# Optimization experiments

Hardware: AMD Instinct MI355X
Metric: run time of the kernel (lower is better)

## Reference

```python
import jax, jax.numpy as jnp
import numpy as np

K = 30  # kNN neighbors (DynamicEdgeConvParams default)

def _knn_idx(x, k):
    # x: [B,N,C] -> indices of k nearest neighbors in feature space, [B,N,k]
    x2 = jnp.sum(x * x, axis=-1)                      # [B,N]
    d = x2[:, :, None] + x2[:, None, :] - 2.0 * jnp.einsum('bnc,bmc->bnm', x, x)
    _, idx = jax.lax.top_k(-d, k)                     # includes self (dist 0)
    return idx

def _edge_conv(x, w0, b0, w1, b1, k):
    # DynamicEdgeConv: kNN on x, edge feat [x_i, x_j - x_i], MLP, max-aggr
    idx = _knn_idx(x, k)                              # [B,N,k]
    xj = jax.vmap(lambda xb, ib: xb[ib])(x, idx)      # [B,N,k,C] gather
    xi = jnp.broadcast_to(x[:, :, None, :], xj.shape)
    e = jnp.concatenate([xi, xj - xi], axis=-1)       # [B,N,k,2C]
    h = jax.nn.relu(jnp.einsum('bnkc,cd->bnkd', e, w0) + b0)
    h = jnp.einsum('bnkc,cd->bnkd', h, w1) + b1
    return jnp.max(h, axis=2)                         # [B,N,out]

def setup_inputs() -> dict:
    key = jax.random.key(0)
    ks = jax.random.split(key, 16)
    def w(k, shape):
        fan_in = shape[0]
        return jax.random.normal(k, shape, jnp.float32) / np.sqrt(fan_in)
    B, N = 16, 2048
    return {
        'pos': jax.random.normal(ks[0], (B, N, 3), jnp.float32),
        'c1_w0': w(ks[1], (6, 64)),   'c1_b0': jnp.zeros((64,), jnp.float32),
        'c1_w1': w(ks[2], (64, 64)),  'c1_b1': jnp.zeros((64,), jnp.float32),
        'c2_w0': w(ks[3], (128, 64)), 'c2_b0': jnp.zeros((64,), jnp.float32),
        'c2_w1': w(ks[4], (64, 64)),  'c2_b1': jnp.zeros((64,), jnp.float32),
        'c3_w0': w(ks[5], (128, 64)), 'c3_b0': jnp.zeros((64,), jnp.float32),
        'c3_w1': w(ks[6], (64, 64)),  'c3_b1': jnp.zeros((64,), jnp.float32),
        'mlp_w0': w(ks[7], (192, 1024)), 'mlp_b0': jnp.zeros((1024,), jnp.float32),
        'mlp_w1': w(ks[8], (1024, 256)), 'mlp_b1': jnp.zeros((256,), jnp.float32),
        'mlp_w2': w(ks[9], (256, 128)),  'mlp_b2': jnp.zeros((128,), jnp.float32),
        'fin_w': w(ks[10], (128, 3)),    'fin_b': jnp.zeros((3,), jnp.float32),
    }

def reference(pos, c1_w0, c1_b0, c1_w1, c1_b1, c2_w0, c2_b0, c2_w1, c2_b1,
              c3_w0, c3_b0, c3_w1, c3_b1, mlp_w0, mlp_b0, mlp_w1, mlp_b1,
              mlp_w2, mlp_b2, fin_w, fin_b):
    x1 = _edge_conv(pos, c1_w0, c1_b0, c1_w1, c1_b1, K)   # [B,N,64]
    x2 = _edge_conv(x1, c2_w0, c2_b0, c2_w1, c2_b1, K)    # [B,N,64]
    x3 = _edge_conv(x2, c3_w0, c3_b0, c3_w1, c3_b1, K)    # [B,N,64]
    h = jnp.concatenate([x1, x2, x3], axis=-1)            # [B,N,192]
    h = jax.nn.relu(h @ mlp_w0 + mlp_b0)
    h = jax.nn.relu(h @ mlp_w1 + mlp_b1)
    h = h @ mlp_w2 + mlp_b2                               # [B,N,128]
    return h @ fin_w + fin_b                              # [B,N,3]
```

## Files before the change

### kernel.cpp

```cpp
#include <hip/hip_runtime.h>
#include <hip/hip_bf16.h>
#include <cfloat>
#include <cstddef>

#define BB 16
#define NN 2048
#define KNN 30
#define MC 8192

using bf16 = __hip_bfloat16;
typedef short short8 __attribute__((ext_vector_type(8)));
typedef float floatx4 __attribute__((ext_vector_type(4)));

constexpr size_t XT_O  = 0;
constexpr size_t NRM_O = XT_O  + (size_t)BB*64*NN;
constexpr size_t A_O   = NRM_O + (size_t)BB*NN;
constexpr size_t U_O   = A_O   + (size_t)BB*NN*64;
constexpr size_t H_O   = U_O   + (size_t)BB*NN*64;
constexpr size_t WS_F  = H_O   + (size_t)BB*NN*192;
constexpr size_t H1C_S = 0;
constexpr size_t H2C_S = 8388608;
constexpr size_t WB_S  = 11534336;
constexpr size_t WB1_S = WB_S + 0;
constexpr size_t WB2_S = WB_S + 196608;
constexpr size_t WB3_S = WB_S + 458752;

__device__ __attribute__((aligned(16))) float g_ws[WS_F];
__device__ int   g_idx[(size_t)BB*NN*KNN];
__device__ int   g_isbf16;

__device__ __forceinline__ float b2f(bf16 x){ return __bfloat162float(x); }
__device__ __forceinline__ float ldi(const void* p, size_t i){
  return g_isbf16 ? b2f(((const bf16*)p)[i]) : ((const float*)p)[i];
}
__device__ __forceinline__ short f2bs(float v){
  bf16 h = __float2bfloat16(v);
  return *reinterpret_cast<short*>(&h);
}
__device__ __forceinline__ float bs2f(short s){
  bf16 h = *reinterpret_cast<bf16*>(&s);
  return __bfloat162float(h);
}
__device__ __forceinline__ unsigned fmono(float x){
  unsigned u = __float_as_uint(x);
  return ((int)u < 0) ? ~u : (u | 0x80000000u);
}

__global__ __launch_bounds__(256) void k_sniff(const unsigned* __restrict__ posw){
  __shared__ int cnt[256];
  const int tid = threadIdx.x;
  int c = 0;
  for(int k=0;k<8;k++){
    unsigned w = posw[tid*8+k];
    unsigned code = (w & 0x7F80u) >> 7;
    if(code >= 119u && code <= 129u) c++;
  }
  cnt[tid] = c; __syncthreads();
  for(int s=128;s>0;s>>=1){ if(tid<s) cnt[tid]+=cnt[tid+s]; __syncthreads(); }
  if(tid==0) g_isbf16 = (cnt[0] > 1024) ? 1 : 0;
}

__global__ __launch_bounds__(256) void k_diag(bf16* __restrict__ out, int n, float v){
  int t = blockIdx.x*256 + threadIdx.x;
  if(t < n) out[t] = __float2bfloat16(v);
}

__global__ __launch_bounds__(256) void k_prep(const void* __restrict__ pos){
  int t = blockIdx.x*256 + threadIdx.x;
  int b = t >> 11, i = t & (NN-1);
  float x = ldi(pos, (size_t)t*3+0), y = ldi(pos, (size_t)t*3+1), z = ldi(pos, (size_t)t*3+2);
  float* Xb = g_ws + XT_O + (size_t)b*64*NN;
  Xb[0*NN+i] = x; Xb[1*NN+i] = y; Xb[2*NN+i] = z;
  g_ws[NRM_O + t] = x*x + y*y + z*z;
}

template<int C, bool EXTIN>
__global__ __launch_bounds__(512, 4) void k_knn_pre(const void* __restrict__ Xin,
    int rowStride, int colOff, const void* __restrict__ W0, const void* __restrict__ b0,
    int xOff){
  constexpr int SM_KNN = 4*NN*4;
  constexpr int SM_PRE = C*64*4*2 + 256;
  constexpr int SMB = SM_KNN > SM_PRE ? SM_KNN : SM_PRE;
  __shared__ __attribute__((aligned(16))) char smem[SMB];
  const int tid = threadIdx.x;
  const int wid = tid >> 6, lane = tid & 63;
  const int bidx = blockIdx.x;

  if(bidx >= 4096){
    float* Wd = (float*)smem;
    float* Wb = Wd + C*64;
    float* bb = Wb + C*64;
    for(int t=tid; t<C*64; t+=512){
      float top = ldi(W0, t), bot = ldi(W0, (size_t)C*64 + t);
      Wd[t] = top - bot; Wb[t] = bot;
    }
    if(tid < 64) bb[tid] = ldi(b0, tid);
    __syncthreads();
    const int pbase = (bidx - 4096)*64 + wid*8;
    float bl = bb[lane];
    float a[8], u[8];
    #pragma unroll
    for(int pp=0;pp<8;pp++){ a[pp] = bl; u[pp] = 0.f; }
    for(int c=0;c<C;c++){
      float wd = Wd[c*64 + lane];
      float wb = Wb[c*64 + lane];
      #pragma unroll
      for(int pp=0;pp<8;pp++){
        float xc;
        if(EXTIN) xc = ldi(Xin, (size_t)(pbase+pp)*rowStride + colOff + c);
        else      xc = g_ws[(size_t)xOff + (size_t)(pbase+pp)*rowStride + colOff + c];
        a[pp] = fmaf(xc, wd, a[pp]);
        u[pp] = fmaf(xc, wb, u[pp]);
      }
    }
    #pragma unroll
    for(int pp=0;pp<8;pp++){
      g_ws[A_O + (size_t)(pbase+pp)*64 + lane] = a[pp];
      g_ws[U_O + (size_t)(pbase+pp)*64 + lane] = u[pp];
    }
    return;
  }

  unsigned (*dlds)[NN] = (unsigned(*)[NN])smem;
  const int b    = bidx >> 8;
  const int i0   = (bidx & 255) * 8;
  const size_t gi0 = (size_t)b*NN + i0;
  const float* Xb  = g_ws + XT_O + (size_t)b*64*NN;
  const float* nrm = g_ws + NRM_O;

  const int j0 = tid*4;
  float4 nj4 = *(const float4*)&nrm[(size_t)b*NN + j0];

  float acc[8][4];
  #pragma unroll
  for(int r=0;r<8;r++)
    #pragma unroll
    for(int s=0;s<4;s++) acc[r][s] = 0.f;

  constexpr int CH  = (C == 3) ? 3 : 2;
  constexpr int NCH = C / CH;
  float4 vb[2][CH];
  #pragma unroll
  for(int cc=0; cc<CH; cc++) vb[0][cc] = *(const float4*)&Xb[(size_t)cc*NN + j0];
  #pragma unroll
  for(int k=0; k<NCH; k++){
    if(k+1 < NCH){
      #pragma unroll
      for(int cc=0; cc<CH; cc++)
        vb[(k+1)&1][cc] = *(const float4*)&Xb[(size_t)((k+1)*CH+cc)*NN + j0];
    }
    #pragma unroll
    for(int cc=0; cc<CH; cc++){
      const int c = k*CH + cc;
      const float4 vj = vb[k&1][cc];
      const float* xr = &Xb[(size_t)c*NN + i0];
      #pragma unroll
      for(int r=0;r<8;r++){
        float xc = xr[r];
        acc[r][0] = fmaf(xc, vj.x, acc[r][0]);
        acc[r][1] = fmaf(xc, vj.y, acc[r][1]);
        acc[r][2] = fmaf(xc, vj.z, acc[r][2]);
        acc[r][3] = fmaf(xc, vj.w, acc[r][3]);
      }
    }
  }

  #pragma unroll
  for(int r=0;r<4;r++){
    float nIr = nrm[gi0 + r];
    uint4 kv;
    kv.x = fmono(fmaf(-2.f, acc[r][0], nIr + nj4.x));
    kv.y = fmono(fmaf(-2.f, acc[r][1], nIr + nj4.y));
    kv.z = fmono(fmaf(-2.f, acc[r][2], nIr + nj4.z));
    kv.w = fmono(fmaf(-2.f, acc[r][3], nIr + nj4.w));
    *(uint4*)&dlds[r][j0] = kv;
  }
  __syncthreads();
  unsigned kk[32];
  if(wid < 4){
    const unsigned* drow = dlds[wid];
    #pragma unroll
    for(int q=0;q<32;q++) kk[q] = drow[lane + (q<<6)];
  }
  __syncthreads();
  #pragma unroll
  for(int r=4;r<8;r++){
    float nIr = nrm[gi0 + r];
    uint4 kv;
    kv.x = fmono(fmaf(-2.f, acc[r][0], nIr + nj4.x));
    kv.y = fmono(fmaf(-2.f, acc[r][1], nIr + nj4.y));
    kv.z = fmono(fmaf(-2.f, acc[r][2], nIr + nj4.z));
    kv.w = fmono(fmaf(-2.f, acc[r][3], nIr + nj4.w));
    *(uint4*)&dlds[r-4][j0] = kv;
  }
  __syncthreads();
  if(wid >= 4){
    const unsigned* drow = dlds[wid-4];
    #pragma unroll
    for(int q=0;q<32;q++) kk[q] = drow[lane + (q<<6)];
  }

  const size_t rowbase = (gi0 + wid)*KNN;

  unsigned lo = 0x80000000u, hi = 0xFFFFFFFFu;
  unsigned T = 0; bool exact = false;
  while(hi - lo > 1u){
    unsigned mid = lo + ((hi - lo) >> 1);
    int tot = 0;
    #pragma unroll
    for(int q=0;q<32;q++) tot += (int)__popcll(__ballot(kk[q] < mid));
    if(tot == KNN){ T = mid; exact = true; break; }
    if(tot < KNN) lo = mid; else hi = mid;
  }

  int base = 0;
  if(exact){
    #pragma unroll
    for(int q=0;q<32;q++){
      bool p = kk[q] < T;
      unsigned long long m = __ballot(p);
      if(p){
        int pos = base + __builtin_amdgcn_mbcnt_hi((unsigned)(m>>32),
                        __builtin_amdgcn_mbcnt_lo((unsigned)m, 0u));
        g_idx[rowbase + pos] = lane + (q<<6);
      }
      base += (int)__popcll(m);
    }
  } else {
    #pragma unroll
    for(int q=0;q<32;q++){
      bool p = kk[q] < lo;
      unsigned long long m = __ballot(p);
      if(p){
        int pos = base + __builtin_amdgcn_mbcnt_hi((unsigned)(m>>32),
                        __builtin_amdgcn_mbcnt_lo((unsigned)m, 0u));
        g_idx[rowbase + pos] = lane + (q<<6);
      }
      base += (int)__popcll(m);
    }
    #pragma unroll
    for(int q=0;q<32;q++){
      bool p = kk[q] == lo;
      unsigned long long m = __ballot(p);
      if(p){
        int pos = base + __builtin_amdgcn_mbcnt_hi((unsigned)(m>>32),
                        __builtin_amdgcn_mbcnt_lo((unsigned)m, 0u));
        if(pos < KNN) g_idx[rowbase + pos] = lane + (q<<6);
      }
      base += (int)__popcll(m);
    }
  }
}

template<bool WRITE_NEXT>
__global__ __launch_bounds__(256) void k_edge_agg(const void* __restrict__ W1,
    const void* __restrict__ b1, int colOff){
  __shared__ short hk_hi[4][32][64] __attribute__((aligned(16)));
  __shared__ short hk_lo[4][32][64] __attribute__((aligned(16)));
  const int tid = threadIdx.x;
  const int wid = tid >> 6, lane = tid & 63;
  const int ml = lane & 15, kgl = lane >> 4;
  short8 wh[2][4], wl[2][4];
  #pragma unroll
  for(int kt=0; kt<2; kt++)
    #pragma unroll
    for(int nt=0; nt<4; nt++)
      #pragma unroll
      for(int j=0; j<8; j++){
        float w = ldi(W1, (size_t)(kt*32 + kgl*8 + j)*64 + nt*16 + ml);
        short hi = f2bs(w);
        wh[kt][nt][j] = hi;
        wl[kt][nt][j] = f2bs(w - bs2f(hi));
      }
  const float bias = ldi(b1, lane);
  hk_hi[wid][30][lane] = 0; hk_hi[wid][31][lane] = 0;
  hk_lo[wid][30][lane] = 0; hk_lo[wid][31][lane] = 0;
  for(int pp=0; pp<4; pp++){
    const int point = blockIdx.x*16 + wid*4 + pp;
    const int b = point >> 11, i = point & (NN-1);
    const float a = g_ws[A_O + (size_t)point*64 + lane];
    const int* ip = g_idx + (size_t)point*KNN;
    const float* Ub = g_ws + U_O + (size_t)b*NN*64;
    int jv = 0;
    if(lane < KNN) jv = ip[lane] & (NN-1);
    #pragma unroll
    for(int kk=0; kk<KNN; kk++){
      int j = __shfl(jv, kk, 64);
      float h = fmaxf(a + Ub[(size_t)j*64 + lane], 0.f);
      short hi = f2bs(h);
      hk_hi[wid][kk][lane] = hi;
      hk_lo[wid][kk][lane] = f2bs(h - bs2f(hi));
    }
    floatx4 acc[2][4];
    #pragma unroll
    for(int t=0;t<2;t++)
      #pragma unroll
      for(int nt=0;nt<4;nt++) acc[t][nt] = (floatx4){0.f,0.f,0.f,0.f};
    #pragma unroll
    for(int t=0;t<2;t++){
      #pragma unroll
      for(int kt=0;kt<2;kt++){
        short8 ah = *(const short8*)&hk_hi[wid][t*16+ml][kt*32 + kgl*8];
        short8 al = *(const short8*)&hk_lo[wid][t*16+ml][kt*32 + kgl*8];
        #pragma unroll
        for(int nt=0;nt<4;nt++){
          acc[t][nt] = __builtin_amdgcn_mfma_f32_16x16x32_bf16(ah, wh[kt][nt], acc[t][nt], 0,0,0);
          acc[t][nt] = __builtin_amdgcn_mfma_f32_16x16x32_bf16(ah, wl[kt][nt], acc[t][nt], 0,0,0);
          acc[t][nt] = __builtin_amdgcn_mfma_f32_16x16x32_bf16(al, wh[kt][nt], acc[t][nt], 0,0,0);
        }
      }
    }
    float cmax[4];
    #pragma unroll
    for(int nt=0;nt<4;nt++){
      float mx = -FLT_MAX;
      #pragma unroll
      for(int t=0;t<2;t++)
        #pragma unroll
        for(int reg=0;reg<4;reg++){
          int m = t*16 + kgl*4 + reg;
          if(m < KNN) mx = fmaxf(mx, acc[t][nt][reg]);
        }
      mx = fmaxf(mx, __shfl_xor(mx, 16, 64));
      mx = fmaxf(mx, __shfl_xor(mx, 32, 64));
      cmax[nt] = mx;
    }
    float r01 = (lane & 16) ? cmax[1] : cmax[0];
    float r23 = (lane & 16) ? cmax[3] : cmax[2];
    float accf = ((lane & 32) ? r23 : r01) + bias;
    g_ws[H_O + (size_t)point*192 + colOff + lane] = accf;
    if(WRITE_NEXT){
      g_ws[XT_O + ((size_t)b*64 + lane)*NN + i] = accf;
      float sq = accf*accf;
      #pragma unroll
      for(int off=32; off>0; off>>=1) sq += __shfl_xor(sq, off, 64);
      if(lane == 0) g_ws[NRM_O + point] = sq;
    }
  }
}

__global__ __launch_bounds__(256) void k_wconv3(const void* __restrict__ W0,
    const void* __restrict__ W1, const void* __restrict__ W2){
  int t = blockIdx.x*256 + threadIdx.x;
  const void* W; int dstOff, rel, lg;
  if(t < 196608)      { W = W0; dstOff = (int)WB1_S; rel = t;          lg = 10; }
  else if(t < 458752) { W = W1; dstOff = (int)WB2_S; rel = t - 196608; lg = 8;  }
  else                { W = W2; dstOff = (int)WB3_S; rel = t - 458752; lg = 7;  }
  int k = rel >> lg, n = rel & ((1<<lg)-1);
  short* dst = (short*)g_ws + dstOff;
  dst[((size_t)((k>>3) << lg) + ((size_t)n))*8 + (k&7)] = f2bs(ldi(W, rel));
}

template<bool ABF16, bool RELU, bool OUTBF16>
__global__ __launch_bounds__(256) void k_mgemm(int aOff, int wOffS, const void* __restrict__ bias,
    int outOff, int Kd, int Nn){
  __shared__ short As[4*128*8] __attribute__((aligned(16)));
  __shared__ short Bs[4*128*8] __attribute__((aligned(16)));
  const int tid = threadIdx.x;
  const int lane = tid & 63, wid = tid >> 6;
  const int waveM = wid >> 1, waveN = wid & 1;
  const int m0 = blockIdx.x * 128, n0 = blockIdx.y * 128;
  const int sm = tid >> 1, skg0 = (tid & 1) * 2;
  const int bn = tid & 127, bkg = tid >> 7;
  const short* Wb = (const short*)g_ws + wOffS;
  floatx4 acc[4][4];
  #pragma unroll
  for(int a=0;a<4;a++)
    #pragma unroll
    for(int bq=0;bq<4;bq++) acc[a][bq] = (floatx4){0.f,0.f,0.f,0.f};

  for(int k0 = 0; k0 < Kd; k0 += 32){
    if(ABF16){
      const short* Ab = (const short*)g_ws + aOff + (size_t)(m0+sm)*Kd + k0 + skg0*8;
      short8 v0 = *(const short8*)Ab;
      short8 v1 = *(const short8*)(Ab+8);
      *(short8*)&As[((skg0  )*128 + sm)*8] = v0;
      *(short8*)&As[((skg0+1)*128 + sm)*8] = v1;
    } else {
      const float* Af = g_ws + aOff + (size_t)(m0+sm)*Kd + k0 + skg0*8;
      float4 f0 = *(const float4*)(Af+0);
      float4 f1 = *(const float4*)(Af+4);
      float4 f2 = *(const float4*)(Af+8);
      float4 f3 = *(const float4*)(Af+12);
      short8 s0, s1;
      s0[0]=f2bs(f0.x); s0[1]=f2bs(f0.y); s0[2]=f2bs(f0.z); s0[3]=f2bs(f0.w);
      s0[4]=f2bs(f1.x); s0[5]=f2bs(f1.y); s0[6]=f2bs(f1.z); s0[7]=f2bs(f1.w);
      s1[0]=f2bs(f2.x); s1[1]=f2bs(f2.y); s1[2]=f2bs(f2.z); s1[3]=f2bs(f2.w);
      s1[4]=f2bs(f3.x); s1[5]=f2bs(f3.y); s1[6]=f2bs(f3.z); s1[7]=f2bs(f3.w);
      *(short8*)&As[((skg0  )*128 + sm)*8] = s0;
      *(short8*)&As[((skg0+1)*128 + sm)*8] = s1;
    }
    #pragma unroll
    for(int i=0;i<2;i++){
      int kg = bkg + i*2;
      const short* src = Wb + ((size_t)((k0>>3) + kg)*Nn + n0 + bn)*8;
      *(short8*)&Bs[(kg*128 + bn)*8] = *(const short8*)src;
    }
    __syncthreads();
    const int kgl = lane >> 4, ml = lane & 15;
    short8 af[4], bf[4];
    #pragma unroll
    for(int t=0;t<4;t++){
      af[t] = *(const short8*)&As[(kgl*128 + waveM*64 + t*16 + ml)*8];
      bf[t] = *(const short8*)&Bs[(kgl*128 + waveN*64 + t*16 + ml)*8];
    }
    #pragma unroll
    for(int tm=0;tm<4;tm++)
      #pragma unroll
      for(int tn=0;tn<4;tn++)
        acc[tm][tn] = __builtin_amdgcn_mfma_f32_16x16x32_bf16(af[tm], bf[tn], acc[tm][tn], 0, 0, 0);
    __syncthreads();
  }
  const int kgl = lane >> 4, ml = lane & 15;
  #pragma unroll
  for(int tn=0;tn<4;tn++){
    int n = n0 + waveN*64 + tn*16 + ml;
    float bv = ldi(bias, n);
    #pragma unroll
    for(int tm=0;tm<4;tm++){
      #pragma unroll
      for(int reg=0;reg<4;reg++){
        int m = m0 + waveM*64 + tm*16 + kgl*4 + reg;
        float v = acc[tm][tn][reg] + bv;
        if(RELU) v = fmaxf(v, 0.f);
        if(OUTBF16) ((short*)g_ws)[(size_t)outOff + (size_t)m*Nn + n] = f2bs(v);
        else        g_ws[(size_t)outOff + (size_t)m*Nn + n] = v;
      }
    }
  }
}

__global__ __launch_bounds__(256) void k_mgemm_fin(int aOff, int wOffS,
    const void* __restrict__ bias, const void* __restrict__ FW, const void* __restrict__ FB,
    void* __restrict__ out, int outPointBase){
  __shared__ short As[4*128*8] __attribute__((aligned(16)));
  __shared__ short Bs[4*128*8] __attribute__((aligned(16)));
  __shared__ float h3[128][129];
  __shared__ float wf[384];
  __shared__ float fb3[3];
  const int Kd = 256, Nn = 128;
  const int tid = threadIdx.x;
  const int lane = tid & 63, wid = tid >> 6;
  const int waveM = wid >> 1, waveN = wid & 1;
  const int m0 = blockIdx.x * 128;
  const int sm = tid >> 1, skg0 = (tid & 1) * 2;
  const int bn = tid & 127, bkg = tid >> 7;
  const short* Wb = (const short*)g_ws + wOffS;
  for(int t=tid; t<384; t+=256) wf[t] = ldi(FW, t);
  if(tid < 3) fb3[tid] = ldi(FB, tid);
  floatx4 acc[4][4];
  #pragma unroll
  for(int a=0;a<4;a++)
    #pragma unroll
    for(int bq=0;bq<4;bq++) acc[a][bq] = (floatx4){0.f,0.f,0.f,0.f};

  for(int k0 = 0; k0 < Kd; k0 += 32){
    const short* Ab = (const short*)g_ws + aOff + (size_t)(m0+sm)*Kd + k0 + skg0*8;
    short8 v0 = *(const short8*)Ab;
    short8 v1 = *(const short8*)(Ab+8);
    *(short8*)&As[((skg0  )*128 + sm)*8] = v0;
    *(short8*)&As[((skg0+1)*128 + sm)*8] = v1;
    #pragma unroll
    for(int i=0;i<2;i++){
      int kg = bkg + i*2;
      const short* src = Wb + ((size_t)((k0>>3) + kg)*Nn + bn)*8;
      *(short8*)&Bs[(kg*128 + bn)*8] = *(const short8*)src;
    }
    __syncthreads();
    const int kgl = lane >> 4, ml = lane & 15;
    short8 af[4], bf[4];
    #pragma unroll
    for(int t=0;t<4;t++){
      af[t] = *(const short8*)&As[(kgl*128 + waveM*64 + t*16 + ml)*8];
      bf[t] = *(const short8*)&Bs[(kgl*128 + waveN*64 + t*16 + ml)*8];
    }
    #pragma unroll
    for(int tm=0;tm<4;tm++)
      #pragma unroll
      for(int tn=0;tn<4;tn++)
        acc[tm][tn] = __builtin_amdgcn_mfma_f32_16x16x32_bf16(af[tm], bf[tn], acc[tm][tn], 0, 0, 0);
    __syncthreads();
  }
  const int kgl = lane >> 4, ml = lane & 15;
  #pragma unroll
  for(int tn=0;tn<4;tn++){
    int n = waveN*64 + tn*16 + ml;
    float bv = ldi(bias, n);
    #pragma unroll
    for(int tm=0;tm<4;tm++){
      #pragma unroll
      for(int reg=0;reg<4;reg++){
        int m = waveM*64 + tm*16 + kgl*4 + reg;
        h3[m][n] = acc[tm][tn][reg] + bv;
      }
    }
  }
  __syncthreads();
  if(tid < 128){
    float a0 = fb3[0], a1 = fb3[1], a2 = fb3[2];
    #pragma unroll 8
    for(int c=0;c<128;c++){
      float x = h3[tid][c];
      a0 = fmaf(x, wf[c*3+0], a0);
      a1 = fmaf(x, wf[c*3+1], a1);
      a2 = fmaf(x, wf[c*3+2], a2);
    }
    size_t o = (size_t)(outPointBase + blockIdx.x*128 + tid)*3;
    if(g_isbf16){
      bf16* ob = (bf16*)out;
      ob[o+0] = __float2bfloat16(a0); ob[o+1] = __float2bfloat16(a1); ob[o+2] = __float2bfloat16(a2);
    } else {
      float* of = (float*)out;
      of[o+0] = a0; of[o+1] = a1; of[o+2] = a2;
    }
  }
}

extern "C" void kernel_launch(void* const* d_in, const int* in_sizes, int n_in,
                              void* d_out, int out_size, void* d_ws, size_t ws_size,
                              hipStream_t stream){
  (void)d_ws; (void)ws_size;
  static const int EXP[21] = {98304, 384,64, 4096,64, 8192,64, 4096,64, 8192,64, 4096,64,
                              196608,1024, 262144,256, 32768,128, 384,3};
  const void* in[21];
  int posmatch = 0;
  bool run = false;
  if(n_in == 21){
    for(int e=0; e<21; e++) posmatch += (in_sizes[e] == EXP[e]) ? 1 : 0;
    if(posmatch == 21){
      for(int e=0; e<21; e++) in[e] = d_in[e];
      run = true;
    } else {
      bool used[21] = {false}; const void* m[21]; bool ok = true;
      for(int e=0; e<21 && ok; e++){
        int hit = -1;
        for(int i2=0; i2<21; i2++)
          if(!used[i2] && in_sizes[i2] == EXP[e]){ hit = i2; break; }
        if(hit < 0) ok = false;
        else { used[hit] = true; m[e] = d_in[hit]; }
      }
      if(ok){ for(int e=0; e<21; e++) in[e] = m[e]; run = true; }
    }
  }
  if(!run){
    float V = 1000.f*(float)n_in + 10.f*(float)posmatch;
    k_diag<<<(out_size+255)/256, 256, 0, stream>>>((bf16*)d_out, out_size, V);
    return;
  }
  const void* pos  = in[0];
  const void* c1w0 = in[1];  const void* c1b0 = in[2];
  const void* c1w1 = in[3];  const void* c1b1 = in[4];
  const void* c2w0 = in[5];  const void* c2b0 = in[6];
  const void* c2w1 = in[7];  const void* c2b1 = in[8];
  const void* c3w0 = in[9];  const void* c3b0 = in[10];
  const void* c3w1 = in[11]; const void* c3b1 = in[12];
  const void* mw0  = in[13]; const void* mb0  = in[14];
  const void* mw1  = in[15]; const void* mb1  = in[16];
  const void* mw2  = in[17]; const void* mb2  = in[18];
  const void* fw   = in[19]; const void* fb   = in[20];

  dim3 b256(256);
  dim3 b512(512);
  k_sniff<<<1, b256, 0, stream>>>((const unsigned*)pos);
  k_prep<<<128, b256, 0, stream>>>(pos);

  k_knn_pre<3,true><<<4608, b512, 0, stream>>>(pos, 3, 0, c1w0, c1b0, 0);
  k_edge_agg<true><<<2048, b256, 0, stream>>>(c1w1, c1b1, 0);

  k_knn_pre<64,false><<<4608, b512, 0, stream>>>(nullptr, 192, 0, c2w0, c2b0, (int)H_O);
  k_edge_agg<true><<<2048, b256, 0, stream>>>(c2w1, c2b1, 64);

  k_knn_pre<64,false><<<4608, b512, 0, stream>>>(nullptr, 192, 64, c3w0, c3b0, (int)H_O);
  k_edge_agg<false><<<2048, b256, 0, stream>>>(c3w1, c3b1, 128);

  k_wconv3<<<1920, b256, 0, stream>>>(mw0, mw1, mw2);

  for(int ch=0; ch<4; ch++){
    int ainOff = (int)(H_O + (size_t)ch*MC*192);
    k_mgemm<false,true ,true ><<<dim3(64,8), b256, 0, stream>>>(ainOff,     (int)WB1_S, mb0, (int)H1C_S, 192, 1024);
    k_mgemm<true ,true ,true ><<<dim3(64,2), b256, 0, stream>>>((int)H1C_S, (int)WB2_S, mb1, (int)H2C_S, 1024, 256);
    k_mgemm_fin<<<64, b256, 0, stream>>>((int)H2C_S, (int)WB3_S, mb2, fw, fb, d_out, ch*MC);
  }
}
```

Before: 1.050 ms.

## Compute kNN distance Gram matrix with split-bf16 MFMA for 64-channel layers

After: 1.335 ms. 1.27x slower.

```diff
diff --git a/kernel.cpp b/kernel.cpp
--- a/kernel.cpp
+++ b/kernel.cpp
@@ -77,8 +77,8 @@
 template<int C, bool EXTIN>
 __global__ __launch_bounds__(512, 4) void k_knn_pre(const void* __restrict__ Xin,
     int rowStride, int colOff, const void* __restrict__ W0, const void* __restrict__ b0,
-    int xOff){
-  constexpr int SM_KNN = 4*NN*4;
+    int xOff, int hiOff, int loOff){
+  constexpr int SM_KNN = (C == 3) ? 4*NN*4 : 8*NN*4;
   constexpr int SM_PRE = C*64*4*2 + 256;
   constexpr int SMB = SM_KNN > SM_PRE ? SM_KNN : SM_PRE;
   __shared__ __attribute__((aligned(16))) char smem[SMB];
@@ -121,38 +121,28 @@
     return;
   }
 
-  unsigned (*dlds)[NN] = (unsigned(*)[NN])smem;
-  const int b    = bidx >> 8;
-  const int i0   = (bidx & 255) * 8;
+  const int knn_id = ((bidx & 7) << 9) | (bidx >> 3);
+  const int b    = knn_id >> 8;
+  const int i0   = (knn_id & 255) * 8;
   const size_t gi0 = (size_t)b*NN + i0;
-  const float* Xb  = g_ws + XT_O + (size_t)b*64*NN;
   const float* nrm = g_ws + NRM_O;
-
-  const int j0 = tid*4;
-  float4 nj4 = *(const float4*)&nrm[(size_t)b*NN + j0];
-
-  float acc[8][4];
-  #pragma unroll
-  for(int r=0;r<8;r++)
-    #pragma unroll
-    for(int s=0;s<4;s++) acc[r][s] = 0.f;
-
-  constexpr int CH  = (C == 3) ? 3 : 2;
-  constexpr int NCH = C / CH;
-  float4 vb[2][CH];
-  #pragma unroll
-  for(int cc=0; cc<CH; cc++) vb[0][cc] = *(const float4*)&Xb[(size_t)cc*NN + j0];
-  #pragma unroll
-  for(int k=0; k<NCH; k++){
-    if(k+1 < NCH){
-      #pragma unroll
-      for(int cc=0; cc<CH; cc++)
-        vb[(k+1)&1][cc] = *(const float4*)&Xb[(size_t)((k+1)*CH+cc)*NN + j0];
-    }
-    #pragma unroll
-    for(int cc=0; cc<CH; cc++){
-      const int c = k*CH + cc;
-      const float4 vj = vb[k&1][cc];
+  const size_t rowbase0 = (gi0 + wid)*KNN;
+
+  unsigned kk[32];
+
+  if constexpr (C == 3){
+    unsigned (*dlds)[NN] = (unsigned(*)[NN])smem;
+    const float* Xb  = g_ws + XT_O + (size_t)b*64*NN;
+    const int j0 = tid*4;
+    float4 nj4 = *(const float4*)&nrm[(size_t)b*NN + j0];
+    float acc[8][4];
+    #pragma unroll
+    for(int r=0;r<8;r++)
+      #pragma unroll
+      for(int s=0;s<4;s++) acc[r][s] = 0.f;
+    #pragma unroll
+    for(int c=0;c<3;c++){
+      float4 vj = *(const float4*)&Xb[(size_t)c*NN + j0];
       const float* xr = &Xb[(size_t)c*NN + i0];
       #pragma unroll
       for(int r=0;r<8;r++){
@@ -163,44 +153,85 @@
         acc[r][3] = fmaf(xc, vj.w, acc[r][3]);
       }
     }
-  }
-
-  #pragma unroll
-  for(int r=0;r<4;r++){
-    float nIr = nrm[gi0 + r];
-    uint4 kv;
-    kv.x = fmono(fmaf(-2.f, acc[r][0], nIr + nj4.x));
-    kv.y = fmono(fmaf(-2.f, acc[r][1], nIr + nj4.y));
-    kv.z = fmono(fmaf(-2.f, acc[r][2], nIr + nj4.z));
-    kv.w = fmono(fmaf(-2.f, acc[r][3], nIr + nj4.w));
-    *(uint4*)&dlds[r][j0] = kv;
-  }
-  __syncthreads();
-  unsigned kk[32];
-  if(wid < 4){
+    #pragma unroll
+    for(int r=0;r<4;r++){
+      float nIr = nrm[gi0 + r];
+      uint4 kv;
+      kv.x = fmono(fmaf(-2.f, acc[r][0], nIr + nj4.x));
+      kv.y = fmono(fmaf(-2.f, acc[r][1], nIr + nj4.y));
+      kv.z = fmono(fmaf(-2.f, acc[r][2], nIr + nj4.z));
+      kv.w = fmono(fmaf(-2.f, acc[r][3], nIr + nj4.w));
+      *(uint4*)&dlds[r][j0] = kv;
+    }
+    __syncthreads();
+    if(wid < 4){
+      const unsigned* drow = dlds[wid];
+      #pragma unroll
+      for(int q=0;q<32;q++) kk[q] = drow[lane + (q<<6)];
+    }
+    __syncthreads();
+    #pragma unroll
+    for(int r=4;r<8;r++){
+      float nIr = nrm[gi0 + r];
+      uint4 kv;
+      kv.x = fmono(fmaf(-2.f, acc[r][0], nIr + nj4.x));
+      kv.y = fmono(fmaf(-2.f, acc[r][1], nIr + nj4.y));
+      kv.z = fmono(fmaf(-2.f, acc[r][2], nIr + nj4.z));
+      kv.w = fmono(fmaf(-2.f, acc[r][3], nIr + nj4.w));
+      *(uint4*)&dlds[r-4][j0] = kv;
+    }
+    __syncthreads();
+    if(wid >= 4){
+      const unsigned* drow = dlds[wid-4];
+      #pragma unroll
+      for(int q=0;q<32;q++) kk[q] = drow[lane + (q<<6)];
+    }
+  } else {
+    unsigned (*dlds)[NN] = (unsigned(*)[NN])smem;
+    const float* Hf = g_ws + H_O;
+    const int ml = lane & 15, kgl = lane >> 4;
+    short8 Ah[2], Al[2];
+    {
+      const size_t abase = (gi0 + (ml & 7))*192;
+      #pragma unroll
+      for(int ks=0; ks<2; ks++){
+        Ah[ks] = *(const short8*)((const unsigned*)Hf + abase + hiOff + ks*16 + kgl*4);
+        Al[ks] = *(const short8*)((const unsigned*)Hf + abase + loOff + ks*16 + kgl*4);
+      }
+    }
+    float nI[8];
+    #pragma unroll
+    for(int r=0;r<8;r++) nI[r] = nrm[gi0 + r];
+    const int jb = wid * 256;
+    #pragma unroll 4
+    for(int t=0; t<16; t++){
+      const int col = jb + t*16 + ml;
+      const size_t bbase = ((size_t)b*NN + col)*192;
+      floatx4 acc = (floatx4){0.f,0.f,0.f,0.f};
+      #pragma unroll
+      for(int ks=0; ks<2; ks++){
+        short8 Bh = *(const short8*)((const unsigned*)Hf + bbase + hiOff + ks*16 + kgl*4);
+        short8 Bl = *(const short8*)((const unsigned*)Hf + bbase + loOff + ks*16 + kgl*4);
+        acc = __builtin_amdgcn_mfma_f32_16x16x32_bf16(Ah[ks], Bh, acc, 0,0,0);
+        acc = __builtin_amdgcn_mfma_f32_16x16x32_bf16(Ah[ks], Bl, acc, 0,0,0);
+        acc = __builtin_amdgcn_mfma_f32_16x16x32_bf16(Al[ks], Bh, acc, 0,0,0);
+      }
+      float nj = nrm[(size_t)b*NN + col];
+      if(kgl < 2){
+        #pragma unroll
+        for(int reg=0; reg<4; reg++){
+          int r = kgl*4 + reg;
+          dlds[r][col] = fmono(fmaf(-2.f, acc[reg], nI[r] + nj));
+        }
+      }
+    }
+    __syncthreads();
     const unsigned* drow = dlds[wid];
     #pragma unroll
     for(int q=0;q<32;q++) kk[q] = drow[lane + (q<<6)];
   }
-  __syncthreads();
-  #pragma unroll
-  for(int r=4;r<8;r++){
-    float nIr = nrm[gi0 + r];
-    uint4 kv;
-    kv.x = fmono(fmaf(-2.f, acc[r][0], nIr + nj4.x));
-    kv.y = fmono(fmaf(-2.f, acc[r][1], nIr + nj4.y));
-    kv.z = fmono(fmaf(-2.f, acc[r][2], nIr + nj4.z));
-    kv.w = fmono(fmaf(-2.f, acc[r][3], nIr + nj4.w));
-    *(uint4*)&dlds[r-4][j0] = kv;
-  }
-  __syncthreads();
-  if(wid >= 4){
-    const unsigned* drow = dlds[wid-4];
-    #pragma unroll
-    for(int q=0;q<32;q++) kk[q] = drow[lane + (q<<6)];
-  }
-
-  const size_t rowbase = (gi0 + wid)*KNN;
+
+  const size_t rowbase = rowbase0;
 
   unsigned lo = 0x80000000u, hi = 0xFFFFFFFFu;
   unsigned T = 0; bool exact = false;
@@ -277,7 +308,7 @@
   hk_lo[wid][30][lane] = 0; hk_lo[wid][31][lane] = 0;
   for(int pp=0; pp<4; pp++){
     const int point = blockIdx.x*16 + wid*4 + pp;
-    const int b = point >> 11, i = point & (NN-1);
+    const int b = point >> 11;
     const float a = g_ws[A_O + (size_t)point*64 + lane];
     const int* ip = g_idx + (size_t)point*KNN;
     const float* Ub = g_ws + U_O + (size_t)b*NN*64;
@@ -330,7 +361,16 @@
     float accf = ((lane & 32) ? r23 : r01) + bias;
     g_ws[H_O + (size_t)point*192 + colOff + lane] = accf;
     if(WRITE_NEXT){
-      g_ws[XT_O + ((size_t)b*64 + lane)*NN + i] = accf;
+      short hhs = f2bs(accf);
+      short hls = f2bs(accf - bs2f(hhs));
+      unsigned hh = (unsigned short)hhs, hl = (unsigned short)hls;
+      unsigned hhp = (unsigned)__shfl_xor((int)hh, 1, 64);
+      unsigned hlp = (unsigned)__shfl_xor((int)hl, 1, 64);
+      if((lane & 1) == 0){
+        unsigned* Hw = (unsigned*)(g_ws + H_O) + (size_t)point*192 + colOff;
+        Hw[64 + (lane>>1)] = hh | (hhp << 16);
+        Hw[96 + (lane>>1)] = hl | (hlp << 16);
+      }
       float sq = accf*accf;
       #pragma unroll
       for(int off=32; off>0; off>>=1) sq += __shfl_xor(sq, off, 64);
@@ -564,13 +604,13 @@
   k_sniff<<<1, b256, 0, stream>>>((const unsigned*)pos);
   k_prep<<<128, b256, 0, stream>>>(pos);
 
-  k_knn_pre<3,true><<<4608, b512, 0, stream>>>(pos, 3, 0, c1w0, c1b0, 0);
+  k_knn_pre<3,true><<<4608, b512, 0, stream>>>(pos, 3, 0, c1w0, c1b0, 0, 0, 0);
   k_edge_agg<true><<<2048, b256, 0, stream>>>(c1w1, c1b1, 0);
 
-  k_knn_pre<64,false><<<4608, b512, 0, stream>>>(nullptr, 192, 0, c2w0, c2b0, (int)H_O);
+  k_knn_pre<64,false><<<4608, b512, 0, stream>>>(nullptr, 192, 0, c2w0, c2b0, (int)H_O, 64, 96);
   k_edge_agg<true><<<2048, b256, 0, stream>>>(c2w1, c2b1, 64);
 
-  k_knn_pre<64,false><<<4608, b512, 0, stream>>>(nullptr, 192, 64, c3w0, c3b0, (int)H_O);
+  k_knn_pre<64,false><<<4608, b512, 0, stream>>>(nullptr, 192, 64, c3w0, c3b0, (int)H_O, 128, 160);
   k_edge_agg<false><<<2048, b256, 0, stream>>>(c3w1, c3b1, 128);
 
   k_wconv3<<<1920, b256, 0, stream>>>(mw0, mw1, mw2);
```
